# Performance work log

Hardware: AMD Instinct MI355X
Metric: run time of the kernel (lower is better)

## Reference

```python
import math
import jax, jax.numpy as jnp
import numpy as np

K, B, T = 6, 8, 12
DIM = 256
DH = 64          # dim_head
NH = 8           # num_heads
G = 8            # offset_groups
INNER = DH * NH  # 512
HALF = INNER // 2  # 256
OFF_D = INNER // G  # 64
HBEV = WBEV = 256
PW = PH = 102.4   # x/y range extents
SCALE = DH ** -0.5
OFF_SCALE = 4.0


def setup_inputs() -> dict:
    key = jax.random.key(0)
    ks = jax.random.split(key, 20)
    w = lambda i, shape: jax.random.normal(ks[i], shape, jnp.float32) * 0.05
    return {
        "dec_embed": jax.random.normal(ks[0], (K, B, T, DIM), jnp.float32),
        "bev_feat": jax.random.normal(ks[1], (B, DIM, HBEV, WBEV), jnp.float32),
        "query_scale": jax.random.uniform(ks[2], (K, B, T, HALF), jnp.float32),
        "ref_points": (jax.random.uniform(ks[3], (K, B, T, 2), jnp.float32) * 2.0 - 1.0) * 51.2,
        "Wq": w(4, (DIM, HALF)), "bq": jnp.zeros((HALF,), jnp.float32),
        "Wk": w(5, (DIM, HALF)),
        "Wv": w(6, (DIM, HALF)),
        "pq_W1": w(7, (HALF, HALF)), "pq_b1": jnp.zeros((HALF,), jnp.float32),
        "pq_W2": w(8, (HALF, HALF)), "pq_b2": jnp.zeros((HALF,), jnp.float32),
        "pk_W1": w(9, (HALF, HALF)), "pk_b1": jnp.zeros((HALF,), jnp.float32),
        "pk_W2": w(10, (HALF, HALF)), "pk_b2": jnp.zeros((HALF,), jnp.float32),
        "off_W1": w(11, (OFF_D // 2, OFF_D)), "off_b1": jnp.zeros((OFF_D,), jnp.float32),
        "off_W2": w(12, (OFF_D, 2)), "off_b2": jnp.zeros((2,), jnp.float32),
        "out_W": w(13, (HALF, DIM)), "out_b": jnp.zeros((DIM,), jnp.float32),
    }


def _grid_sample(im, grid):
    """F.grid_sample, bilinear, padding_mode='zeros', align_corners=False.
    im: (B,C,H,W), grid: (B,Hg,Wg,2) with (x,y) in [-1,1]. Returns (B,C,Hg,Wg)."""
    Bn, C, Hh, Ww = im.shape
    gx, gy = grid[..., 0], grid[..., 1]
    ix = ((gx + 1.0) * Ww - 1.0) * 0.5
    iy = ((gy + 1.0) * Hh - 1.0) * 0.5
    ix0 = jnp.floor(ix)
    iy0 = jnp.floor(iy)
    wx = (ix - ix0)[:, None]  # (B,1,Hg,Wg)
    wy = (iy - iy0)[:, None]
    imf = im.reshape(Bn, C, Hh * Ww)

    def gather(xq, yq):
        valid = (xq >= 0) & (xq < Ww) & (yq >= 0) & (yq < Hh)
        idx = (jnp.clip(yq, 0, Hh - 1) * Ww + jnp.clip(xq, 0, Ww - 1)).astype(jnp.int32)
        v = jnp.take_along_axis(imf, idx.reshape(Bn, 1, -1), axis=2)
        v = v.reshape(Bn, C, *xq.shape[1:])
        return v * valid[:, None].astype(im.dtype)

    v00 = gather(ix0, iy0)
    v01 = gather(ix0 + 1, iy0)
    v10 = gather(ix0, iy0 + 1)
    v11 = gather(ix0 + 1, iy0 + 1)
    return (v00 * (1 - wx) * (1 - wy) + v01 * wx * (1 - wy)
            + v10 * (1 - wx) * wy + v11 * wx * wy)


def _sine_embed(pos, hidden=256, temp=40.0):
    """DAB-DETR style sine embedding for 2D positions. pos: (...,2) -> (...,hidden)."""
    half = hidden // 2
    dim_t = jnp.arange(half, dtype=pos.dtype)
    dim_t = temp ** (2.0 * jnp.floor(dim_t / 2.0) / half)
    sc = 2.0 * math.pi
    ex = pos[..., 0, None] * sc / dim_t
    ey = pos[..., 1, None] * sc / dim_t

    def interleave(e):
        return jnp.stack((jnp.sin(e[..., 0::2]), jnp.cos(e[..., 1::2])), axis=-1).reshape(*e.shape[:-1], -1)

    return jnp.concatenate((interleave(ey), interleave(ex)), axis=-1)


def reference(dec_embed, bev_feat, query_scale, ref_points,
              Wq, bq, Wk, Wv,
              pq_W1, pq_b1, pq_W2, pq_b2,
              pk_W1, pk_b1, pk_W2, pk_b2,
              off_W1, off_b1, off_W2, off_b2,
              out_W, out_b):
    de = dec_embed.transpose(1, 0, 2, 3)     # (B,K,T,D)
    qs = query_scale.transpose(1, 0, 2, 3)   # (B,K,T,256)
    rp = ref_points.transpose(1, 0, 2, 3)    # (B,K,T,2)
    Bn, Kn, Tn = de.shape[:3]

    con_q = de @ Wq + bq                                    # (B,K,T,256)
    oin = con_q.reshape(Bn, Kn, Tn, G, OFF_D // 2)          # (B,K,T,G,32)
    off = jax.nn.gelu(oin @ off_W1 + off_b1, approximate=False)
    off = jnp.tanh(off @ off_W2 + off_b2) * OFF_SCALE       # (B,K,T,G,2)

    vgrid = rp[..., None, :] + off                          # (B,K,T,G,2)
    vgrid = vgrid.reshape(Bn, Kn * Tn, G, 2)
    norm = jnp.array([2.0 / PW, 2.0 / PH], vgrid.dtype)
    vgrid_scaled = vgrid * norm                             # ref_from_Q normalization

    con_k_map = jnp.einsum('bchw,cd->bdhw', bev_feat, Wk)   # 1x1 conv, no bias
    v_map = jnp.einsum('bchw,cd->bdhw', bev_feat, Wv)
    con_k = _grid_sample(con_k_map, vgrid_scaled)           # (B,256,KT,G)
    v = _grid_sample(v_map, vgrid_scaled)                   # (B,256,KT,G)

    ref_scaled = rp * norm                                  # (B,K,T,2)
    qse = _sine_embed(ref_scaled)                           # (B,K,T,256)
    pos_q = (jax.nn.relu(qse @ pq_W1 + pq_b1) @ pq_W2 + pq_b2) * qs
    kse = _sine_embed(vgrid_scaled)                         # (B,KT,G,256)
    pos_k = jax.nn.relu(kse @ pk_W1 + pk_b1) @ pk_W2 + pk_b2

    BS = Bn * Kn * Tn
    dh = HALF // NH  # 32 per-head content dim
    cq = con_q.reshape(BS, 1, NH, dh)
    pq = pos_q.reshape(BS, 1, NH, dh)
    ck = con_k.transpose(0, 2, 3, 1).reshape(BS, G, NH, dh)
    pk = pos_k.reshape(BS, G, NH, dh)
    vv = v.transpose(0, 2, 3, 1).reshape(BS, G, NH, dh)

    q = jnp.concatenate([cq, pq], -1).transpose(0, 2, 1, 3) * SCALE  # (BS,NH,1,64)
    k = jnp.concatenate([ck, pk], -1).transpose(0, 2, 1, 3)          # (BS,NH,G,64)
    vv = vv.transpose(0, 2, 1, 3)                                    # (BS,NH,G,32)

    sim = jnp.einsum('bhid,bhjd->bhij', q, k)               # (BS,NH,1,G)
    attn = jax.nn.softmax(sim, axis=-1)
    out = jnp.einsum('bhij,bhjd->bhid', attn, vv)           # (BS,NH,1,32)

    out = out.transpose(0, 2, 1, 3).reshape(Bn, Kn, Tn, HALF).transpose(1, 0, 2, 3)
    out = out @ out_W + out_b                               # (K,B,T,D)
    return dec_embed + out
```

## Files before the change

kernel.cpp:

```cpp
#include <hip/hip_runtime.h>
#include <math.h>

#define NK 6
#define NB 8
#define NT 12
#define D 256
#define NG 8
#define NHD 8
#define HW 256
#define NQ (NK*NB*NT)

__global__ __launch_bounds__(256)
void dca_kernel(const float* __restrict__ dec_embed,
                const float* __restrict__ bev_feat,
                const float* __restrict__ query_scale,
                const float* __restrict__ ref_points,
                const float* __restrict__ Wq,     const float* __restrict__ bq,
                const float* __restrict__ Wk,     const float* __restrict__ Wv,
                const float* __restrict__ pq_W1,  const float* __restrict__ pq_b1,
                const float* __restrict__ pq_W2,  const float* __restrict__ pq_b2,
                const float* __restrict__ pk_W1,  const float* __restrict__ pk_b1,
                const float* __restrict__ pk_W2,  const float* __restrict__ pk_b2,
                const float* __restrict__ off_W1, const float* __restrict__ off_b1,
                const float* __restrict__ off_W2, const float* __restrict__ off_b2,
                const float* __restrict__ out_W,  const float* __restrict__ out_b,
                float* __restrict__ out)
{
    __shared__ float de[D];
    __shared__ float conq[D];
    __shared__ float qse[D];
    __shared__ float tmp1[D];
    __shared__ float posq[D];
    __shared__ float oatt[D];
    __shared__ float h1[NG][64];
    __shared__ float gxy[NG][2];
    __shared__ float sim[NHD][NG];
    __shared__ float bufA[NG][D];
    __shared__ float bufB[NG][D];
    __shared__ float conk[NG][D];
    __shared__ float vmat[NG][D];

    const int tid = threadIdx.x;
    const int q   = blockIdx.x;
    const int bb  = (q / NT) % NB;

    const float NORM = 0.01953125f;
    const float TWO_PI = 6.28318530717958647692f;
    const float L2_40_OVER_64 = 5.32192809488736234787f / 64.0f;

    de[tid] = dec_embed[(size_t)q * D + tid];
    __syncthreads();

    {
        float acc = bq[tid];
        #pragma unroll 8
        for (int i = 0; i < D; ++i) acc += de[i] * Wq[i * D + tid];
        conq[tid] = acc;
    }
    __syncthreads();

    for (int idx = tid; idx < NG * 64; idx += 256) {
        int g = idx >> 6, j = idx & 63;
        float acc = off_b1[j];
        #pragma unroll 8
        for (int i = 0; i < 32; ++i) acc += conq[g * 32 + i] * off_W1[i * 64 + j];
        h1[g][j] = 0.5f * acc * (1.0f + erff(acc * 0.70710678118654752440f));
    }
    __syncthreads();

    if (tid < NG * 2) {
        int g = tid >> 1, c = tid & 1;
        float acc = off_b2[c];
        #pragma unroll 8
        for (int j = 0; j < 64; ++j) acc += h1[g][j] * off_W2[j * 2 + c];
        float off = tanhf(acc) * 4.0f;
        float rp  = ref_points[(size_t)q * 2 + c];
        gxy[g][c] = (rp + off) * NORM;
    }
    __syncthreads();

    {
        const float* bevb = bev_feat + (size_t)bb * D * HW * HW;
        const int c = tid;
        const float* ch = bevb + (size_t)c * HW * HW;
        #pragma unroll
        for (int g = 0; g < NG; ++g) {
            float gx = gxy[g][0], gy = gxy[g][1];
            float ix = ((gx + 1.0f) * HW - 1.0f) * 0.5f;
            float iy = ((gy + 1.0f) * HW - 1.0f) * 0.5f;
            float fx0 = floorf(ix), fy0 = floorf(iy);
            float wx = ix - fx0, wy = iy - fy0;
            int x0 = (int)fx0, y0 = (int)fy0;
            bool xin0 = (x0 >= 0) && (x0 < HW);
            bool xin1 = (x0 + 1 >= 0) && (x0 + 1 < HW);
            bool yin0 = (y0 >= 0) && (y0 < HW);
            bool yin1 = (y0 + 1 >= 0) && (y0 + 1 < HW);
            float v00 = 0.f, v01 = 0.f, v10 = 0.f, v11 = 0.f;
            if (yin0) {
                if (xin0) v00 = ch[y0 * HW + x0];
                if (xin1) v01 = ch[y0 * HW + x0 + 1];
            }
            if (yin1) {
                if (xin0) v10 = ch[(y0 + 1) * HW + x0];
                if (xin1) v11 = ch[(y0 + 1) * HW + x0 + 1];
            }
            bufA[g][c] = v00 * (1.f - wx) * (1.f - wy) + v01 * wx * (1.f - wy)
                       + v10 * (1.f - wx) * wy        + v11 * wx * wy;
        }
        {
            float rx = ref_points[(size_t)q * 2 + 0] * NORM;
            float ry = ref_points[(size_t)q * 2 + 1] * NORM;
            int j = tid;
            float pos = (j < 128) ? ry : rx;
            int m = (j & 127) >> 1;
            float freq = TWO_PI / exp2f((float)m * L2_40_OVER_64);
            float e = pos * freq;
            qse[j] = (j & 1) ? cosf(e) : sinf(e);
        }
        #pragma unroll
        for (int g = 0; g < NG; ++g) {
            int j = tid;
            float pos = (j < 128) ? gxy[g][1] : gxy[g][0];
            int m = (j & 127) >> 1;
            float freq = TWO_PI / exp2f((float)m * L2_40_OVER_64);
            float e = pos * freq;
            bufB[g][j] = (j & 1) ? cosf(e) : sinf(e);
        }
    }
    __syncthreads();

    {
        float accK[NG], accV[NG];
        #pragma unroll
        for (int g = 0; g < NG; ++g) { accK[g] = 0.f; accV[g] = 0.f; }
        #pragma unroll 4
        for (int i = 0; i < D; ++i) {
            float wk = Wk[i * D + tid];
            float wv = Wv[i * D + tid];
            #pragma unroll
            for (int g = 0; g < NG; ++g) {
                float s = bufA[g][i];
                accK[g] += s * wk;
                accV[g] += s * wv;
            }
        }
        #pragma unroll
        for (int g = 0; g < NG; ++g) { conk[g][tid] = accK[g]; vmat[g][tid] = accV[g]; }
    }
    __syncthreads();

    {
        float acc[NG + 1];
        float biask = pk_b1[tid];
        #pragma unroll
        for (int g = 0; g < NG; ++g) acc[g] = biask;
        acc[NG] = pq_b1[tid];
        #pragma unroll 4
        for (int i = 0; i < D; ++i) {
            float wk1 = pk_W1[i * D + tid];
            float wq1 = pq_W1[i * D + tid];
            #pragma unroll
            for (int g = 0; g < NG; ++g) acc[g] += bufB[g][i] * wk1;
            acc[NG] += qse[i] * wq1;
        }
        #pragma unroll
        for (int g = 0; g < NG; ++g) bufA[g][tid] = fmaxf(acc[g], 0.f);
        tmp1[tid] = fmaxf(acc[NG], 0.f);
    }
    __syncthreads();

    {
        float acc[NG + 1];
        float biask = pk_b2[tid];
        #pragma unroll
        for (int g = 0; g < NG; ++g) acc[g] = biask;
        acc[NG] = pq_b2[tid];
        #pragma unroll 4
        for (int i = 0; i < D; ++i) {
            float wk2 = pk_W2[i * D + tid];
            float wq2 = pq_W2[i * D + tid];
            #pragma unroll
            for (int g = 0; g < NG; ++g) acc[g] += bufA[g][i] * wk2;
            acc[NG] += tmp1[i] * wq2;
        }
        #pragma unroll
        for (int g = 0; g < NG; ++g) bufB[g][tid] = acc[g];
        posq[tid] = acc[NG] * query_scale[(size_t)q * D + tid];
    }
    __syncthreads();

    if (tid < NHD * NG) {
        int h = tid >> 3, g = tid & 7;
        float s = 0.f;
        #pragma unroll 8
        for (int d = 0; d < 32; ++d) {
            s += conq[h * 32 + d] * conk[g][h * 32 + d];
            s += posq[h * 32 + d] * bufB[g][h * 32 + d];
        }
        sim[h][g] = s * 0.125f;
    }
    __syncthreads();

    if (tid < NHD) {
        int h = tid;
        float mx = sim[h][0];
        for (int g = 1; g < NG; ++g) mx = fmaxf(mx, sim[h][g]);
        float ex[NG], sum = 0.f;
        #pragma unroll
        for (int g = 0; g < NG; ++g) { ex[g] = expf(sim[h][g] - mx); sum += ex[g]; }
        float inv = 1.0f / sum;
        #pragma unroll
        for (int g = 0; g < NG; ++g) sim[h][g] = ex[g] * inv;
    }
    __syncthreads();

    {
        int h = tid >> 5, d = tid & 31;
        float o = 0.f;
        #pragma unroll
        for (int g = 0; g < NG; ++g) o += sim[h][g] * vmat[g][h * 32 + d];
        oatt[tid] = o;
    }
    __syncthreads();

    {
        float acc = out_b[tid];
        #pragma unroll 8
        for (int i = 0; i < D; ++i) acc += oatt[i] * out_W[i * D + tid];
        out[(size_t)q * D + tid] = acc + de[tid];
    }
}

extern "C" void kernel_launch(void* const* d_in, const int* in_sizes, int n_in,
                              void* d_out, int out_size, void* d_ws, size_t ws_size,
                              hipStream_t stream) {
    const float* dec_embed   = (const float*)d_in[0];
    const float* bev_feat    = (const float*)d_in[1];
    const float* query_scale = (const float*)d_in[2];
    const float* ref_points  = (const float*)d_in[3];
    const float* Wq     = (const float*)d_in[4];
    const float* bq     = (const float*)d_in[5];
    const float* Wk     = (const float*)d_in[6];
    const float* Wv     = (const float*)d_in[7];
    const float* pq_W1  = (const float*)d_in[8];
    const float* pq_b1  = (const float*)d_in[9];
    const float* pq_W2  = (const float*)d_in[10];
    const float* pq_b2  = (const float*)d_in[11];
    const float* pk_W1  = (const float*)d_in[12];
    const float* pk_b1  = (const float*)d_in[13];
    const float* pk_W2  = (const float*)d_in[14];
    const float* pk_b2  = (const float*)d_in[15];
    const float* off_W1 = (const float*)d_in[16];
    const float* off_b1 = (const float*)d_in[17];
    const float* off_W2 = (const float*)d_in[18];
    const float* off_b2 = (const float*)d_in[19];
    const float* out_W  = (const float*)d_in[20];
    const float* out_b  = (const float*)d_in[21];
    float* out = (float*)d_out;

    dca_kernel<<<NQ, 256, 0, stream>>>(dec_embed, bev_feat, query_scale, ref_points,
                                       Wq, bq, Wk, Wv,
                                       pq_W1, pq_b1, pq_W2, pq_b2,
                                       pk_W1, pk_b1, pk_W2, pk_b2,
                                       off_W1, off_b1, off_W2, off_b2,
                                       out_W, out_b, out);
}
```

Baseline: 759.9 us.

## Split fused per-query kernel into front, batched GEMM, and attention kernels

Splits the monolithic per-query kernel into three launches. The first computes per-query projections, offsets, bilinear samples and sine embeddings into a workspace. The second runs the key/value and positional-key MLP GEMMs over tiles of 16 sampled rows, reusing each weight load across more rows with float4 shared reads. The third does the softmax attention and output projection. This cuts redundant weight traffic per row and spreads the per-query serial chain across more blocks, at the cost of workspace round-trips and extra launches. It falls back to the old kernel if the workspace is too small.

```diff
diff --git a/kernel.cpp b/kernel.cpp
--- a/kernel.cpp
+++ b/kernel.cpp
@@ -9,6 +9,295 @@
 #define NHD 8
 #define HW 256
 #define NQ (NK*NB*NT)
+#define NR (NQ*NG)
+#define TR 16
+
+#define WS_CONQ 0
+#define WS_POSQ (WS_CONQ + NQ*D)
+#define WS_SAMP (WS_POSQ + NQ*D)
+#define WS_KSE  (WS_SAMP + NR*D)
+#define WS_CONK (WS_KSE  + NR*D)
+#define WS_VMAT (WS_CONK + NR*D)
+#define WS_POSK (WS_VMAT + NR*D)
+#define WS_TOTAL (WS_POSK + NR*D)
+
+__global__ __launch_bounds__(256)
+void k1_front(const float* __restrict__ dec_embed,
+              const float* __restrict__ bev_feat,
+              const float* __restrict__ query_scale,
+              const float* __restrict__ ref_points,
+              const float* __restrict__ Wq,     const float* __restrict__ bq,
+              const float* __restrict__ pq_W1,  const float* __restrict__ pq_b1,
+              const float* __restrict__ pq_W2,  const float* __restrict__ pq_b2,
+              const float* __restrict__ off_W1, const float* __restrict__ off_b1,
+              const float* __restrict__ off_W2, const float* __restrict__ off_b2,
+              float* __restrict__ ws)
+{
+    __shared__ float de[D];
+    __shared__ float conq[D];
+    __shared__ float qse[D];
+    __shared__ float tmp1[D];
+    __shared__ float h1[NG][64];
+    __shared__ float gxy[NG][2];
+
+    const int tid = threadIdx.x;
+    const int q   = blockIdx.x;
+    const int bb  = (q / NT) % NB;
+
+    const float NORM = 0.01953125f;
+    const float TWO_PI = 6.28318530717958647692f;
+    const float L2_40_OVER_64 = 5.32192809488736234787f / 64.0f;
+
+    de[tid] = dec_embed[(size_t)q * D + tid];
+    __syncthreads();
+
+    {
+        float acc = bq[tid];
+        #pragma unroll 8
+        for (int i = 0; i < D; ++i) acc += de[i] * Wq[i * D + tid];
+        conq[tid] = acc;
+        ws[WS_CONQ + (size_t)q * D + tid] = acc;
+    }
+    __syncthreads();
+
+    for (int idx = tid; idx < NG * 64; idx += 256) {
+        int g = idx >> 6, j = idx & 63;
+        float acc = off_b1[j];
+        #pragma unroll 8
+        for (int i = 0; i < 32; ++i) acc += conq[g * 32 + i] * off_W1[i * 64 + j];
+        h1[g][j] = 0.5f * acc * (1.0f + erff(acc * 0.70710678118654752440f));
+    }
+    __syncthreads();
+
+    if (tid < NG * 2) {
+        int g = tid >> 1, c = tid & 1;
+        float acc = off_b2[c];
+        #pragma unroll 8
+        for (int j = 0; j < 64; ++j) acc += h1[g][j] * off_W2[j * 2 + c];
+        float off = tanhf(acc) * 4.0f;
+        float rp  = ref_points[(size_t)q * 2 + c];
+        gxy[g][c] = (rp + off) * NORM;
+    }
+    {
+        float rx = ref_points[(size_t)q * 2 + 0] * NORM;
+        float ry = ref_points[(size_t)q * 2 + 1] * NORM;
+        int j = tid;
+        float pos = (j < 128) ? ry : rx;
+        int m = (j & 127) >> 1;
+        float freq = TWO_PI / exp2f((float)m * L2_40_OVER_64);
+        float e = pos * freq;
+        qse[j] = (j & 1) ? cosf(e) : sinf(e);
+    }
+    __syncthreads();
+
+    {
+        const float* ch = bev_feat + ((size_t)bb * D + tid) * HW * HW;
+        #pragma unroll
+        for (int g = 0; g < NG; ++g) {
+            float gx = gxy[g][0], gy = gxy[g][1];
+            float ix = ((gx + 1.0f) * HW - 1.0f) * 0.5f;
+            float iy = ((gy + 1.0f) * HW - 1.0f) * 0.5f;
+            float fx0 = floorf(ix), fy0 = floorf(iy);
+            float wx = ix - fx0, wy = iy - fy0;
+            int x0 = (int)fx0, y0 = (int)fy0;
+            bool xin0 = (x0 >= 0) && (x0 < HW);
+            bool xin1 = (x0 + 1 >= 0) && (x0 + 1 < HW);
+            bool yin0 = (y0 >= 0) && (y0 < HW);
+            bool yin1 = (y0 + 1 >= 0) && (y0 + 1 < HW);
+            float v00 = 0.f, v01 = 0.f, v10 = 0.f, v11 = 0.f;
+            if (yin0) {
+                if (xin0) v00 = ch[y0 * HW + x0];
+                if (xin1) v01 = ch[y0 * HW + x0 + 1];
+            }
+            if (yin1) {
+                if (xin0) v10 = ch[(y0 + 1) * HW + x0];
+                if (xin1) v11 = ch[(y0 + 1) * HW + x0 + 1];
+            }
+            float val = v00 * (1.f - wx) * (1.f - wy) + v01 * wx * (1.f - wy)
+                      + v10 * (1.f - wx) * wy        + v11 * wx * wy;
+            ws[WS_SAMP + (size_t)(q * NG + g) * D + tid] = val;
+        }
+        int m = (tid & 127) >> 1;
+        float freq = TWO_PI / exp2f((float)m * L2_40_OVER_64);
+        #pragma unroll
+        for (int g = 0; g < NG; ++g) {
+            float pos = (tid < 128) ? gxy[g][1] : gxy[g][0];
+            float e = pos * freq;
+            ws[WS_KSE + (size_t)(q * NG + g) * D + tid] = (tid & 1) ? cosf(e) : sinf(e);
+        }
+    }
+
+    {
+        float a1 = pq_b1[tid];
+        #pragma unroll 8
+        for (int i = 0; i < D; ++i) a1 += qse[i] * pq_W1[i * D + tid];
+        tmp1[tid] = fmaxf(a1, 0.f);
+    }
+    __syncthreads();
+    {
+        float a2 = pq_b2[tid];
+        #pragma unroll 8
+        for (int i = 0; i < D; ++i) a2 += tmp1[i] * pq_W2[i * D + tid];
+        ws[WS_POSQ + (size_t)q * D + tid] = a2 * query_scale[(size_t)q * D + tid];
+    }
+}
+
+__global__ __launch_bounds__(256)
+void k2_gemms(const float* __restrict__ Wk, const float* __restrict__ Wv,
+              const float* __restrict__ pk_W1, const float* __restrict__ pk_b1,
+              const float* __restrict__ pk_W2, const float* __restrict__ pk_b2,
+              float* __restrict__ ws)
+{
+    __shared__ float sIn[TR][D];
+    __shared__ float sH[TR][D];
+    const int tid = threadIdx.x;
+    const int b = blockIdx.x;
+
+    if (b < NR / TR) {
+        const int r0 = b * TR;
+        const float* samp = ws + WS_SAMP;
+        for (int idx = tid; idx < TR * D; idx += 256)
+            sIn[idx >> 8][idx & 255] = samp[(size_t)(r0 + (idx >> 8)) * D + (idx & 255)];
+        __syncthreads();
+
+        float accK[TR], accV[TR];
+        #pragma unroll
+        for (int r = 0; r < TR; ++r) { accK[r] = 0.f; accV[r] = 0.f; }
+
+        #pragma unroll 2
+        for (int i = 0; i < D; i += 4) {
+            float wk0 = Wk[(i + 0) * D + tid], wk1 = Wk[(i + 1) * D + tid];
+            float wk2 = Wk[(i + 2) * D + tid], wk3 = Wk[(i + 3) * D + tid];
+            float wv0 = Wv[(i + 0) * D + tid], wv1 = Wv[(i + 1) * D + tid];
+            float wv2 = Wv[(i + 2) * D + tid], wv3 = Wv[(i + 3) * D + tid];
+            #pragma unroll
+            for (int r = 0; r < TR; ++r) {
+                float4 s = *(const float4*)&sIn[r][i];
+                accK[r] += s.x * wk0 + s.y * wk1 + s.z * wk2 + s.w * wk3;
+                accV[r] += s.x * wv0 + s.y * wv1 + s.z * wv2 + s.w * wv3;
+            }
+        }
+        float* conk = ws + WS_CONK;
+        float* vmat = ws + WS_VMAT;
+        #pragma unroll
+        for (int r = 0; r < TR; ++r) {
+            conk[(size_t)(r0 + r) * D + tid] = accK[r];
+            vmat[(size_t)(r0 + r) * D + tid] = accV[r];
+        }
+    } else {
+        const int r0 = (b - NR / TR) * TR;
+        const float* kse = ws + WS_KSE;
+        for (int idx = tid; idx < TR * D; idx += 256)
+            sIn[idx >> 8][idx & 255] = kse[(size_t)(r0 + (idx >> 8)) * D + (idx & 255)];
+        __syncthreads();
+
+        float acc[TR];
+        float b1 = pk_b1[tid];
+        #pragma unroll
+        for (int r = 0; r < TR; ++r) acc[r] = b1;
+
+        #pragma unroll 2
+        for (int i = 0; i < D; i += 4) {
+            float w0 = pk_W1[(i + 0) * D + tid], w1 = pk_W1[(i + 1) * D + tid];
+            float w2 = pk_W1[(i + 2) * D + tid], w3 = pk_W1[(i + 3) * D + tid];
+            #pragma unroll
+            for (int r = 0; r < TR; ++r) {
+                float4 s = *(const float4*)&sIn[r][i];
+                acc[r] += s.x * w0 + s.y * w1 + s.z * w2 + s.w * w3;
+            }
+        }
+        #pragma unroll
+        for (int r = 0; r < TR; ++r) sH[r][tid] = fmaxf(acc[r], 0.f);
+        __syncthreads();
+
+        float b2 = pk_b2[tid];
+        #pragma unroll
+        for (int r = 0; r < TR; ++r) acc[r] = b2;
+        #pragma unroll 2
+        for (int i = 0; i < D; i += 4) {
+            float w0 = pk_W2[(i + 0) * D + tid], w1 = pk_W2[(i + 1) * D + tid];
+            float w2 = pk_W2[(i + 2) * D + tid], w3 = pk_W2[(i + 3) * D + tid];
+            #pragma unroll
+            for (int r = 0; r < TR; ++r) {
+                float4 s = *(const float4*)&sH[r][i];
+                acc[r] += s.x * w0 + s.y * w1 + s.z * w2 + s.w * w3;
+            }
+        }
+        float* posk = ws + WS_POSK;
+        #pragma unroll
+        for (int r = 0; r < TR; ++r)
+            posk[(size_t)(r0 + r) * D + tid] = acc[r];
+    }
+}
+
+__global__ __launch_bounds__(256)
+void k3_attn(const float* __restrict__ dec_embed,
+             const float* __restrict__ out_W, const float* __restrict__ out_b,
+             const float* __restrict__ ws,
+             float* __restrict__ out)
+{
+    __shared__ float cq[D];
+    __shared__ float pq[D];
+    __shared__ float oatt[D];
+    __shared__ float ck[NG][D];
+    __shared__ float pk[NG][D];
+    __shared__ float vv[NG][D];
+    __shared__ float sim[NHD][NG];
+
+    const int tid = threadIdx.x;
+    const int q = blockIdx.x;
+
+    cq[tid] = ws[WS_CONQ + (size_t)q * D + tid];
+    pq[tid] = ws[WS_POSQ + (size_t)q * D + tid];
+    #pragma unroll
+    for (int g = 0; g < NG; ++g) {
+        ck[g][tid] = ws[WS_CONK + (size_t)(q * NG + g) * D + tid];
+        pk[g][tid] = ws[WS_POSK + (size_t)(q * NG + g) * D + tid];
+        vv[g][tid] = ws[WS_VMAT + (size_t)(q * NG + g) * D + tid];
+    }
+    __syncthreads();
+
+    if (tid < NHD * NG) {
+        int h = tid >> 3, g = tid & 7;
+        float s = 0.f;
+        #pragma unroll 8
+        for (int d = 0; d < 32; ++d) {
+            s += cq[h * 32 + d] * ck[g][h * 32 + d];
+            s += pq[h * 32 + d] * pk[g][h * 32 + d];
+        }
+        sim[h][g] = s * 0.125f;
+    }
+    __syncthreads();
+
+    if (tid < NHD) {
+        int h = tid;
+        float mx = sim[h][0];
+        for (int g = 1; g < NG; ++g) mx = fmaxf(mx, sim[h][g]);
+        float ex[NG], sum = 0.f;
+        #pragma unroll
+        for (int g = 0; g < NG; ++g) { ex[g] = expf(sim[h][g] - mx); sum += ex[g]; }
+        float inv = 1.0f / sum;
+        #pragma unroll
+        for (int g = 0; g < NG; ++g) sim[h][g] = ex[g] * inv;
+    }
+    __syncthreads();
+
+    {
+        int h = tid >> 5, d = tid & 31;
+        float o = 0.f;
+        #pragma unroll
+        for (int g = 0; g < NG; ++g) o += sim[h][g] * vv[g][h * 32 + d];
+        oatt[tid] = o;
+    }
+    __syncthreads();
+
+    {
+        float acc = out_b[tid];
+        #pragma unroll 8
+        for (int i = 0; i < D; ++i) acc += oatt[i] * out_W[i * D + tid];
+        out[(size_t)q * D + tid] = acc + dec_embed[(size_t)q * D + tid];
+    }
+}
 
 __global__ __launch_bounds__(256)
 void dca_kernel(const float* __restrict__ dec_embed,
@@ -50,7 +339,6 @@
 
     de[tid] = dec_embed[(size_t)q * D + tid];
     __syncthreads();
-
     {
         float acc = bq[tid];
         #pragma unroll 8
@@ -58,7 +346,6 @@
         conq[tid] = acc;
     }
     __syncthreads();
-
     for (int idx = tid; idx < NG * 64; idx += 256) {
         int g = idx >> 6, j = idx & 63;
         float acc = off_b1[j];
@@ -67,7 +354,6 @@
         h1[g][j] = 0.5f * acc * (1.0f + erff(acc * 0.70710678118654752440f));
     }
     __syncthreads();
-
     if (tid < NG * 2) {
         int g = tid >> 1, c = tid & 1;
         float acc = off_b2[c];
@@ -78,7 +364,6 @@
         gxy[g][c] = (rp + off) * NORM;
     }
     __syncthreads();
-
     {
         const float* bevb = bev_feat + (size_t)bb * D * HW * HW;
         const int c = tid;
@@ -128,7 +413,6 @@
         }
     }
     __syncthreads();
-
     {
         float accK[NG], accV[NG];
         #pragma unroll
@@ -148,7 +432,6 @@
         for (int g = 0; g < NG; ++g) { conk[g][tid] = accK[g]; vmat[g][tid] = accV[g]; }
     }
     __syncthreads();
-
     {
         float acc[NG + 1];
         float biask = pk_b1[tid];
@@ -168,7 +451,6 @@
         tmp1[tid] = fmaxf(acc[NG], 0.f);
     }
     __syncthreads();
-
     {
         float acc[NG + 1];
         float biask = pk_b2[tid];
@@ -188,7 +470,6 @@
         posq[tid] = acc[NG] * query_scale[(size_t)q * D + tid];
     }
     __syncthreads();
-
     if (tid < NHD * NG) {
         int h = tid >> 3, g = tid & 7;
         float s = 0.f;
@@ -200,7 +481,6 @@
         sim[h][g] = s * 0.125f;
     }
     __syncthreads();
-
     if (tid < NHD) {
         int h = tid;
         float mx = sim[h][0];
@@ -213,7 +493,6 @@
         for (int g = 0; g < NG; ++g) sim[h][g] = ex[g] * inv;
     }
     __syncthreads();
-
     {
         int h = tid >> 5, d = tid & 31;
         float o = 0.f;
@@ -222,7 +501,6 @@
         oatt[tid] = o;
     }
     __syncthreads();
-
     {
         float acc = out_b[tid];
         #pragma unroll 8
@@ -257,11 +535,20 @@
     const float* out_W  = (const float*)d_in[20];
     const float* out_b  = (const float*)d_in[21];
     float* out = (float*)d_out;
-
-    dca_kernel<<<NQ, 256, 0, stream>>>(dec_embed, bev_feat, query_scale, ref_points,
-                                       Wq, bq, Wk, Wv,
-                                       pq_W1, pq_b1, pq_W2, pq_b2,
-                                       pk_W1, pk_b1, pk_W2, pk_b2,
-                                       off_W1, off_b1, off_W2, off_b2,
-                                       out_W, out_b, out);
+    float* ws = (float*)d_ws;
+
+    if (ws_size >= (size_t)WS_TOTAL * sizeof(float)) {
+        k1_front<<<NQ, 256, 0, stream>>>(dec_embed, bev_feat, query_scale, ref_points,
+                                         Wq, bq, pq_W1, pq_b1, pq_W2, pq_b2,
+                                         off_W1, off_b1, off_W2, off_b2, ws);
+        k2_gemms<<<2 * (NR / TR), 256, 0, stream>>>(Wk, Wv, pk_W1, pk_b1, pk_W2, pk_b2, ws);
+        k3_attn<<<NQ, 256, 0, stream>>>(dec_embed, out_W, out_b, ws, out);
+    } else {
+        dca_kernel<<<NQ, 256, 0, stream>>>(dec_embed, bev_feat, query_scale, ref_points,
+                                           Wq, bq, Wk, Wv,
+                                           pq_W1, pq_b1, pq_W2, pq_b2,
+                                           pk_W1, pk_b1, pk_W2, pk_b2,
+                                           off_W1, off_b1, off_W2, off_b2,
+                                           out_W, out_b, out);
+    }
 }
```

New measurement: 795.4 us. 4.7% more time.
